# Performance work log

Measured on AMD Instinct MI355X. Metric: run time of the kernel, lower is better.

## Reference

```python
import jax, jax.numpy as jnp
import numpy as np


def _hard_sigmoid(x):
    # Keras ConvLSTM2D default recurrent_activation
    return jnp.clip(0.2 * x + 0.5, 0.0, 1.0)


def _conv(x, w):
    # NHWC input, HWIO kernel, SAME padding, stride 1
    return jax.lax.conv_general_dilated(
        x, w, (1, 1), 'SAME', dimension_numbers=('NHWC', 'HWIO', 'NHWC'))


def _convlstm(seq, h, c, k, rk, b):
    # seq: [B, T, H, W, Cin]; h, c: [B, H, W, F]
    # k: [kh, kw, Cin, 4F], rk: [kh, kw, F, 4F], b: [4F]
    def step(carry, x):
        h, c = carry
        z = _conv(x, k) + _conv(h, rk) + b  # [B,H,W,4F]
        zi, zf, zc, zo = jnp.split(z, 4, axis=-1)
        i = _hard_sigmoid(zi)
        f = _hard_sigmoid(zf)
        o = _hard_sigmoid(zo)
        c = f * c + i * jnp.tanh(zc)
        h = o * jnp.tanh(c)
        return (h, c), None
    (h, c), _ = jax.lax.scan(step, (h, c), jnp.swapaxes(seq, 0, 1))
    return h, c


def setup_inputs() -> dict:
    key = jax.random.key(0)
    ks = jax.random.split(key, 14)
    B, T, H, W, Cin, F, K = 32, 1, 64, 64, 1, 64, 3
    s = 0.05
    inp = {
        'input_': jax.random.normal(ks[0], (B, T, H, W, Cin), jnp.float32),
        'h0': jax.random.normal(ks[1], (B, H, W, F), jnp.float32) * s,
        'c0': jax.random.normal(ks[2], (B, H, W, F), jnp.float32) * s,
        'h1': jax.random.normal(ks[3], (B, H, W, F), jnp.float32) * s,
        'c1': jax.random.normal(ks[4], (B, H, W, F), jnp.float32) * s,
        'k0': jax.random.normal(ks[5], (K, K, Cin, 4 * F), jnp.float32) * s,
        'rk0': jax.random.normal(ks[6], (K, K, F, 4 * F), jnp.float32) * s,
        'b0': jnp.zeros((4 * F,), jnp.float32),
        'k1': jax.random.normal(ks[7], (K, K, F, 4 * F), jnp.float32) * s,
        'rk1': jax.random.normal(ks[8], (K, K, F, 4 * F), jnp.float32) * s,
        'b1': jnp.zeros((4 * F,), jnp.float32),
        'cw': jax.random.normal(ks[9], (1, 1, F, 1), jnp.float32) * s,
        'cb': jnp.zeros((1,), jnp.float32),
    }
    return inp


def reference(input_, h0, c0, h1, c1, k0, rk0, b0, k1, rk1, b1, cw, cb):
    # Layer 0 consumes the input frame sequence (T=1)
    h0n, c0n = _convlstm(input_, h0, c0, k0, rk0, b0)
    # Layer 1 consumes layer-0's last hidden state as its (length-1) input
    h1n, c1n = _convlstm(h0n[:, None], h1, c1, k1, rk1, b1)
    frames = _conv(h1n, cw) + cb  # 1x1 conv head -> [B,H,W,1]
    return frames, h0n, c0n, h1n, c1n
```

## Files before the change

kernel.cpp:

```cpp
#include <hip/hip_runtime.h>
#include <hip/hip_bf16.h>

typedef short s16;
typedef __attribute__((ext_vector_type(8))) short bf16x8;
typedef __attribute__((ext_vector_type(4))) float f32x4;

__device__ __forceinline__ s16 f2bf(float f) {
  unsigned u = __builtin_bit_cast(unsigned, f);
  unsigned r = (u + 0x7FFFu + ((u >> 16) & 1u)) >> 16;
  return (s16)r;
}

__device__ __forceinline__ float hsig(float x) {
  return fminf(fmaxf(0.2f * x + 0.5f, 0.0f), 1.0f);
}

__global__ void wprep_kernel(const float* __restrict__ rk0, const float* __restrict__ k1,
                             const float* __restrict__ rk1, const float* __restrict__ k0,
                             s16* __restrict__ w0q, s16* __restrict__ w1q,
                             s16* __restrict__ w2q, s16* __restrict__ k0t) {
  int idx = blockIdx.x * 256 + threadIdx.x;
  const int n1 = 9 * 2 * 4 * 4 * 512;
  if (idx < 3 * n1) {
    int which = idx / n1;
    int i = idx - which * n1;
    int e    = i & 7;
    int lane = (i >> 3) & 63;
    int g    = (i >> 9) & 3;
    int j    = (i >> 11) & 3;
    int k    = (i >> 13) & 1;
    int tap  = i >> 14;
    int l15 = lane & 15, l4 = lane >> 4;
    int ic = k * 32 + l4 * 8 + e;
    int oc = j * 64 + g * 16 + l15;
    const float* src = (which == 0) ? rk0 : (which == 1) ? k1 : rk1;
    s16* dst = (which == 0) ? w0q : (which == 1) ? w1q : w2q;
    dst[i] = f2bf(src[(tap * 64 + ic) * 256 + oc]);
  } else if (idx < 3 * n1 + 8192) {
    int r = idx - 3 * n1;
    int kk = r & 31;
    int oc = r >> 5;
    k0t[r] = (kk < 9) ? f2bf(k0[kk * 256 + oc]) : (s16)0;
  }
}

#define PXS 66
#define ROWSZ (PXS * 64)
#define ASZ (4 * ROWSZ)

template <bool F32>
__device__ __forceinline__ bf16x8 load_conv8(const void* src, long off) {
  if constexpr (F32) {
    const float* p = (const float*)src + off;
    float4 v0 = *reinterpret_cast<const float4*>(p);
    float4 v1 = *reinterpret_cast<const float4*>(p + 4);
    bf16x8 r;
    r[0] = f2bf(v0.x); r[1] = f2bf(v0.y); r[2] = f2bf(v0.z); r[3] = f2bf(v0.w);
    r[4] = f2bf(v1.x); r[5] = f2bf(v1.y); r[6] = f2bf(v1.z); r[7] = f2bf(v1.w);
    return r;
  } else {
    return *reinterpret_cast<const bf16x8*>((const s16*)src + off);
  }
}

template <bool F32>
__device__ __forceinline__ void stage_src(s16* a_lds, const void* src, int b, int y0, int tid) {
  #pragma unroll
  for (int i = 0; i < 4; ++i) {
    int c   = tid + i * 512;
    int row = c >> 9;
    int px  = (c >> 3) & 63;
    int cb  = c & 7;
    int y   = y0 - 1 + row;
    int xp  = px + 1;
    bf16x8 v = {};
    if ((unsigned)y < 64u)
      v = load_conv8<F32>(src, ((long)(b * 64 + y) * 64 + px) * 64 + cb * 8);
    *reinterpret_cast<bf16x8*>(a_lds + (row * PXS + xp) * 64 + ((cb ^ (xp & 7)) * 8)) = v;
  }
  if (tid < 64) {
    int row = tid >> 4;
    int xp  = ((tid >> 3) & 1) ? 65 : 0;
    int cb  = tid & 7;
    bf16x8 z = {};
    *reinterpret_cast<bf16x8*>(a_lds + (row * PXS + xp) * 64 + cb * 8) = z;
  }
}

template <int NSRC, bool XPATH, bool S0F32, bool S1F32>
__global__ __launch_bounds__(512, 4) void cell_kernel(
    const void* __restrict__ src0,
    const void* __restrict__ src1,
    const s16* __restrict__ w0,
    const s16* __restrict__ w1,
    const float* __restrict__ xin,
    const s16* __restrict__ k0t,
    const float* __restrict__ bias,
    const float* __restrict__ c_old,
    float* __restrict__ h_out,
    float* __restrict__ c_out,
    s16* __restrict__ hb_out)
{
  __shared__ __align__(16) s16 a_lds[NSRC * ASZ];
  __shared__ float x_lds[XPATH ? 256 : 1];

  const int tid = threadIdx.x;
  const int b  = blockIdx.x >> 5;
  const int y0 = (blockIdx.x & 31) << 1;

  stage_src<S0F32>(a_lds, src0, b, y0, tid);
  if (NSRC == 2) stage_src<S1F32>(a_lds + ASZ, src1, b, y0, tid);
  if (XPATH) {
    if (tid < 256) {
      int row = tid >> 6, px = tid & 63;
      int y = y0 - 1 + row;
      x_lds[tid] = ((unsigned)y < 64u) ? xin[(b * 64 + y) * 64 + px] : 0.0f;
    }
  }
  __syncthreads();

  const int wave = tid >> 6;
  const int lane = tid & 63;
  const int g    = wave & 3;
  const int mh   = wave >> 2;
  const int l15  = lane & 15;
  const int l4   = lane >> 4;

  constexpr int NST = NSRC * 18;

  f32x4 acc[4][4] = {};

  if (XPATH) {
    bf16x8 bx[4];
    #pragma unroll
    for (int j = 0; j < 4; ++j) {
      int oc = j * 64 + g * 16 + l15;
      bx[j] = *reinterpret_cast<const bf16x8*>(k0t + oc * 32 + l4 * 8);
    }
    #pragma unroll
    for (int m = 0; m < 4; ++m) {
      int px = m * 16 + l15;
      bf16x8 ax = {};
      #pragma unroll
      for (int j = 0; j < 8; ++j) {
        int t = l4 * 8 + j;
        if (t < 9) {
          int dyt = t / 3, dxt = t - dyt * 3;
          int xx = px + dxt - 1;
          float xv = ((unsigned)xx < 64u) ? x_lds[(mh + dyt) * 64 + xx] : 0.0f;
          ax[j] = f2bf(xv);
        }
      }
      #pragma unroll
      for (int j = 0; j < 4; ++j)
        acc[m][j] = __builtin_amdgcn_mfma_f32_16x16x32_bf16(ax, bx[j], acc[m][j], 0, 0, 0);
    }
  }

  const int wl_off = g * 512 + lane * 8;
  auto loadW = [&](bf16x8 (&wf)[4], int u) {
    int si = (NSRC == 2 && u >= 18) ? 1 : 0;
    const s16* wp = (si ? w1 : w0) + (u - 18 * si) * 8192 + wl_off;
    #pragma unroll
    for (int j = 0; j < 4; ++j)
      wf[j] = *reinterpret_cast<const bf16x8*>(wp + j * 2048);
  };

  auto doStage = [&](const bf16x8 (&wf)[4], int u) {
    int si = (NSRC == 2 && u >= 18) ? 1 : 0;
    int uu = u - 18 * si;
    int tap = uu >> 1, kk = uu & 1;
    int dy = tap / 3, dx = tap - dy * 3;
    const char* lb = (const char*)a_lds + (si * ASZ + (mh + dy) * ROWSZ) * 2;
    #pragma unroll
    for (int m = 0; m < 4; ++m) {
      int xq   = m * 16 + l15 + dx;
      int boff = xq * 128 + (((kk << 6) | (l4 << 4)) ^ ((xq & 7) << 4));
      bf16x8 a = *reinterpret_cast<const bf16x8*>(lb + boff);
      #pragma unroll
      for (int j = 0; j < 4; ++j)
        acc[m][j] = __builtin_amdgcn_mfma_f32_16x16x32_bf16(a, wf[j], acc[m][j], 0, 0, 0);
    }
  };

  bf16x8 wfA[4], wfB[4];
  loadW(wfA, 0);
  loadW(wfB, 1);
  #pragma unroll
  for (int u = 0; u < NST; u += 2) {
    doStage(wfA, u);
    if (u + 2 < NST) loadW(wfA, u + 2);
    doStage(wfB, u + 1);
    if (u + 3 < NST) loadW(wfB, u + 3);
  }

  float bi[4];
  #pragma unroll
  for (int j = 0; j < 4; ++j) bi[j] = bias[j * 64 + g * 16 + l15];

  const int pix_base = b * 4096 + y0 * 64;
  const int f = g * 16 + l15;
  #pragma unroll
  for (int m = 0; m < 4; ++m) {
    #pragma unroll
    for (int r = 0; r < 4; ++r) {
      int pl = mh * 64 + m * 16 + l4 * 4 + r;
      int off = (pix_base + pl) * 64 + f;
      float zi = acc[m][0][r] + bi[0];
      float zf = acc[m][1][r] + bi[1];
      float zc = acc[m][2][r] + bi[2];
      float zo = acc[m][3][r] + bi[3];
      float ig = hsig(zi), fg = hsig(zf), og = hsig(zo);
      float cn = fg * c_old[off] + ig * tanhf(zc);
      float hn = og * tanhf(cn);
      c_out[off] = cn;
      h_out[off] = hn;
      if (hb_out) hb_out[off] = f2bf(hn);
    }
  }
}

__global__ void frames_kernel(const float* __restrict__ h, const float* __restrict__ cw,
                              const float* __restrict__ cbp, float* __restrict__ out) {
  int tid = blockIdx.x * 256 + threadIdx.x;
  int p  = tid >> 2;
  int fc = (tid & 3) * 16;
  const float4* hp = reinterpret_cast<const float4*>(h + p * 64 + fc);
  const float4* wp = reinterpret_cast<const float4*>(cw + fc);
  float s = 0.0f;
  #pragma unroll
  for (int i = 0; i < 4; ++i) {
    float4 v = hp[i];
    float4 w = wp[i];
    s += v.x * w.x + v.y * w.y + v.z * w.z + v.w * w.w;
  }
  s += __shfl_xor(s, 1);
  s += __shfl_xor(s, 2);
  if ((tid & 3) == 0) out[p] = s + cbp[0];
}

extern "C" void kernel_launch(void* const* d_in, const int* in_sizes, int n_in,
                              void* d_out, int out_size, void* d_ws, size_t ws_size,
                              hipStream_t stream) {
  const float* x   = (const float*)d_in[0];
  const float* h0  = (const float*)d_in[1];
  const float* c0  = (const float*)d_in[2];
  const float* h1  = (const float*)d_in[3];
  const float* c1  = (const float*)d_in[4];
  const float* k0  = (const float*)d_in[5];
  const float* rk0 = (const float*)d_in[6];
  const float* b0  = (const float*)d_in[7];
  const float* k1  = (const float*)d_in[8];
  const float* rk1 = (const float*)d_in[9];
  const float* b1  = (const float*)d_in[10];
  const float* cw  = (const float*)d_in[11];
  const float* cbp = (const float*)d_in[12];

  float* out    = (float*)d_out;
  float* frames = out;
  float* h0n    = out + 131072;
  float* c0n    = out + 131072 + 8388608;
  float* h1n    = out + 131072 + 2 * 8388608;
  float* c1n    = out + 131072 + 3 * 8388608;

  char* ws = (char*)d_ws;
  const size_t SZ_H = 16777216;
  s16* h0nb = (s16*)(ws + 0 * SZ_H);
  s16* w0q  = (s16*)(ws + 1 * SZ_H);
  s16* w1q  = (s16*)(ws + 1 * SZ_H + 1 * 294912);
  s16* w2q  = (s16*)(ws + 1 * SZ_H + 2 * 294912);
  s16* k0t  = (s16*)(ws + 1 * SZ_H + 3 * 294912);

  wprep_kernel<<<1760, 256, 0, stream>>>(rk0, k1, rk1, k0, w0q, w1q, w2q, k0t);

  cell_kernel<1, true, true, false><<<1024, 512, 0, stream>>>(
      h0, nullptr, w0q, nullptr, x, k0t, b0, c0, h0n, c0n, h0nb);

  cell_kernel<2, false, false, true><<<1024, 512, 0, stream>>>(
      h0nb, h1, w1q, w2q, nullptr, nullptr, b1, c1, h1n, c1n, nullptr);

  frames_kernel<<<2048, 256, 0, stream>>>(h1n, cw, cbp, frames);
}
```

Measured before the change: 206.5 us.

## Switch cell conv GEMM to 32x32x16 MFMA with remapped wave tiling

```diff
diff --git a/kernel.cpp b/kernel.cpp
--- a/kernel.cpp
+++ b/kernel.cpp
@@ -3,7 +3,7 @@
 
 typedef short s16;
 typedef __attribute__((ext_vector_type(8))) short bf16x8;
-typedef __attribute__((ext_vector_type(4))) float f32x4;
+typedef __attribute__((ext_vector_type(16))) float f32x16;
 
 __device__ __forceinline__ s16 f2bf(float f) {
   unsigned u = __builtin_bit_cast(unsigned, f);
@@ -20,26 +20,27 @@
                              s16* __restrict__ w0q, s16* __restrict__ w1q,
                              s16* __restrict__ w2q, s16* __restrict__ k0t) {
   int idx = blockIdx.x * 256 + threadIdx.x;
-  const int n1 = 9 * 2 * 4 * 4 * 512;
+  const int n1 = 18 * 8192;
   if (idx < 3 * n1) {
     int which = idx / n1;
     int i = idx - which * n1;
     int e    = i & 7;
     int lane = (i >> 3) & 63;
-    int g    = (i >> 9) & 3;
-    int j    = (i >> 11) & 3;
-    int k    = (i >> 13) & 1;
-    int tap  = i >> 14;
-    int l15 = lane & 15, l4 = lane >> 4;
-    int ic = k * 32 + l4 * 8 + e;
-    int oc = j * 64 + g * 16 + l15;
+    int g2   = (i >> 9) & 1;
+    int j    = (i >> 10) & 3;
+    int k16  = (i >> 12) & 1;
+    int t2   = i >> 13;
+    int l31 = lane & 31, lh = lane >> 5;
+    int tap = t2 >> 1, k32 = t2 & 1;
+    int ic = k32 * 32 + k16 * 16 + lh * 8 + e;
+    int oc = j * 64 + g2 * 32 + l31;
     const float* src = (which == 0) ? rk0 : (which == 1) ? k1 : rk1;
     s16* dst = (which == 0) ? w0q : (which == 1) ? w1q : w2q;
     dst[i] = f2bf(src[(tap * 64 + ic) * 256 + oc]);
-  } else if (idx < 3 * n1 + 8192) {
+  } else if (idx < 3 * n1 + 4096) {
     int r = idx - 3 * n1;
-    int kk = r & 31;
-    int oc = r >> 5;
+    int kk = r & 15;
+    int oc = r >> 4;
     k0t[r] = (kk < 9) ? f2bf(k0[kk * 256 + oc]) : (s16)0;
   }
 }
@@ -121,102 +122,94 @@
 
   const int wave = tid >> 6;
   const int lane = tid & 63;
-  const int g    = wave & 3;
-  const int mh   = wave >> 2;
-  const int l15  = lane & 15;
-  const int l4   = lane >> 4;
-
-  constexpr int NST = NSRC * 18;
-
-  f32x4 acc[4][4] = {};
+  const int g2   = wave & 1;
+  const int mq   = wave >> 1;
+  const int l31  = lane & 31;
+  const int lh   = lane >> 5;
+  const int xbase = (mq & 1) * 32 + l31;
+  const int rowb  = mq >> 1;
+
+  constexpr int NSTEP = NSRC * 36;
+
+  f32x16 acc[4] = {};
 
   if (XPATH) {
-    bf16x8 bx[4];
     #pragma unroll
     for (int j = 0; j < 4; ++j) {
-      int oc = j * 64 + g * 16 + l15;
-      bx[j] = *reinterpret_cast<const bf16x8*>(k0t + oc * 32 + l4 * 8);
-    }
-    #pragma unroll
-    for (int m = 0; m < 4; ++m) {
-      int px = m * 16 + l15;
+      int oc = j * 64 + g2 * 32 + l31;
+      bf16x8 bx = *reinterpret_cast<const bf16x8*>(k0t + oc * 16 + lh * 8);
       bf16x8 ax = {};
       #pragma unroll
-      for (int j = 0; j < 8; ++j) {
-        int t = l4 * 8 + j;
+      for (int e = 0; e < 8; ++e) {
+        int t = lh * 8 + e;
         if (t < 9) {
           int dyt = t / 3, dxt = t - dyt * 3;
-          int xx = px + dxt - 1;
-          float xv = ((unsigned)xx < 64u) ? x_lds[(mh + dyt) * 64 + xx] : 0.0f;
-          ax[j] = f2bf(xv);
+          int xx = xbase + dxt - 1;
+          float xv = ((unsigned)xx < 64u) ? x_lds[(rowb + dyt) * 64 + xx] : 0.0f;
+          ax[e] = f2bf(xv);
         }
       }
-      #pragma unroll
-      for (int j = 0; j < 4; ++j)
-        acc[m][j] = __builtin_amdgcn_mfma_f32_16x16x32_bf16(ax, bx[j], acc[m][j], 0, 0, 0);
+      acc[j] = __builtin_amdgcn_mfma_f32_32x32x16_bf16(ax, bx, acc[j], 0, 0, 0);
     }
   }
 
-  const int wl_off = g * 512 + lane * 8;
-  auto loadW = [&](bf16x8 (&wf)[4], int u) {
+  const int wl_off = g2 * 512 + lane * 8;
+  auto loadW = [&](bf16x8 (&wf)[4], int s) {
+    int u = s >> 1, k16 = s & 1;
     int si = (NSRC == 2 && u >= 18) ? 1 : 0;
-    const s16* wp = (si ? w1 : w0) + (u - 18 * si) * 8192 + wl_off;
+    const s16* wp = (si ? w1 : w0) + (u - 18 * si) * 8192 + k16 * 4096 + wl_off;
     #pragma unroll
     for (int j = 0; j < 4; ++j)
-      wf[j] = *reinterpret_cast<const bf16x8*>(wp + j * 2048);
+      wf[j] = *reinterpret_cast<const bf16x8*>(wp + j * 1024);
   };
 
-  auto doStage = [&](const bf16x8 (&wf)[4], int u) {
+  auto doStep = [&](const bf16x8 (&wf)[4], int s) {
+    int u = s >> 1, k16 = s & 1;
     int si = (NSRC == 2 && u >= 18) ? 1 : 0;
     int uu = u - 18 * si;
-    int tap = uu >> 1, kk = uu & 1;
+    int tap = uu >> 1, k32 = uu & 1;
     int dy = tap / 3, dx = tap - dy * 3;
-    const char* lb = (const char*)a_lds + (si * ASZ + (mh + dy) * ROWSZ) * 2;
+    int xq = xbase + dx;
+    int cb = k32 * 4 + k16 * 2 + lh;
+    int boff = xq * 128 + ((cb ^ (xq & 7)) * 16);
+    const char* lb = (const char*)a_lds + (si * ASZ + (rowb + dy) * ROWSZ) * 2;
+    bf16x8 a = *reinterpret_cast<const bf16x8*>(lb + boff);
     #pragma unroll
-    for (int m = 0; m < 4; ++m) {
-      int xq   = m * 16 + l15 + dx;
-      int boff = xq * 128 + (((kk << 6) | (l4 << 4)) ^ ((xq & 7) << 4));
-      bf16x8 a = *reinterpret_cast<const bf16x8*>(lb + boff);
-      #pragma unroll
-      for (int j = 0; j < 4; ++j)
-        acc[m][j] = __builtin_amdgcn_mfma_f32_16x16x32_bf16(a, wf[j], acc[m][j], 0, 0, 0);
-    }
+    for (int j = 0; j < 4; ++j)
+      acc[j] = __builtin_amdgcn_mfma_f32_32x32x16_bf16(a, wf[j], acc[j], 0, 0, 0);
   };
 
   bf16x8 wfA[4], wfB[4];
   loadW(wfA, 0);
   loadW(wfB, 1);
   #pragma unroll
-  for (int u = 0; u < NST; u += 2) {
-    doStage(wfA, u);
-    if (u + 2 < NST) loadW(wfA, u + 2);
-    doStage(wfB, u + 1);
-    if (u + 3 < NST) loadW(wfB, u + 3);
+  for (int s = 0; s < NSTEP; s += 2) {
+    doStep(wfA, s);
+    if (s + 2 < NSTEP) loadW(wfA, s + 2);
+    doStep(wfB, s + 1);
+    if (s + 3 < NSTEP) loadW(wfB, s + 3);
   }
 
   float bi[4];
   #pragma unroll
-  for (int j = 0; j < 4; ++j) bi[j] = bias[j * 64 + g * 16 + l15];
+  for (int j = 0; j < 4; ++j) bi[j] = bias[j * 64 + g2 * 32 + l31];
 
   const int pix_base = b * 4096 + y0 * 64;
-  const int f = g * 16 + l15;
-  #pragma unroll
-  for (int m = 0; m < 4; ++m) {
-    #pragma unroll
-    for (int r = 0; r < 4; ++r) {
-      int pl = mh * 64 + m * 16 + l4 * 4 + r;
-      int off = (pix_base + pl) * 64 + f;
-      float zi = acc[m][0][r] + bi[0];
-      float zf = acc[m][1][r] + bi[1];
-      float zc = acc[m][2][r] + bi[2];
-      float zo = acc[m][3][r] + bi[3];
-      float ig = hsig(zi), fg = hsig(zf), og = hsig(zo);
-      float cn = fg * c_old[off] + ig * tanhf(zc);
-      float hn = og * tanhf(cn);
-      c_out[off] = cn;
-      h_out[off] = hn;
-      if (hb_out) hb_out[off] = f2bf(hn);
-    }
+  const int f = g2 * 32 + l31;
+  #pragma unroll
+  for (int r = 0; r < 16; ++r) {
+    int pxl = (r & 3) + 8 * (r >> 2) + 4 * lh;
+    int off = (pix_base + mq * 32 + pxl) * 64 + f;
+    float zi = acc[0][r] + bi[0];
+    float zf = acc[1][r] + bi[1];
+    float zc = acc[2][r] + bi[2];
+    float zo = acc[3][r] + bi[3];
+    float ig = hsig(zi), fg = hsig(zf), og = hsig(zo);
+    float cn = fg * c_old[off] + ig * tanhf(zc);
+    float hn = og * tanhf(cn);
+    c_out[off] = cn;
+    h_out[off] = hn;
+    if (hb_out) hb_out[off] = f2bf(hn);
   }
 }
 
@@ -271,7 +264,7 @@
   s16* w2q  = (s16*)(ws + 1 * SZ_H + 2 * 294912);
   s16* k0t  = (s16*)(ws + 1 * SZ_H + 3 * 294912);
 
-  wprep_kernel<<<1760, 256, 0, stream>>>(rk0, k1, rk1, k0, w0q, w1q, w2q, k0t);
+  wprep_kernel<<<1744, 256, 0, stream>>>(rk0, k1, rk1, k0, w0q, w1q, w2q, k0t);
 
   cell_kernel<1, true, true, false><<<1024, 512, 0, stream>>>(
       h0, nullptr, w0q, nullptr, x, k0t, b0, c0, h0n, c0n, h0nb);
```

Result: slower. 288.7 us (+39.8%).

## Split cell tile across 16 waves with halved accumulators and rolled loop

Applied to the files above, without the earlier changes.

```diff
diff --git a/kernel.cpp b/kernel.cpp
--- a/kernel.cpp
+++ b/kernel.cpp
@@ -20,7 +20,7 @@
                              s16* __restrict__ w0q, s16* __restrict__ w1q,
                              s16* __restrict__ w2q, s16* __restrict__ k0t) {
   int idx = blockIdx.x * 256 + threadIdx.x;
-  const int n1 = 9 * 2 * 4 * 4 * 512;
+  const int n1 = 18 * 8192;
   if (idx < 3 * n1) {
     int which = idx / n1;
     int i = idx - which * n1;
@@ -66,8 +66,8 @@
 template <bool F32>
 __device__ __forceinline__ void stage_src(s16* a_lds, const void* src, int b, int y0, int tid) {
   #pragma unroll
-  for (int i = 0; i < 4; ++i) {
-    int c   = tid + i * 512;
+  for (int i = 0; i < 2; ++i) {
+    int c   = tid + i * 1024;
     int row = c >> 9;
     int px  = (c >> 3) & 63;
     int cb  = c & 7;
@@ -88,7 +88,7 @@
 }
 
 template <int NSRC, bool XPATH, bool S0F32, bool S1F32>
-__global__ __launch_bounds__(512, 4) void cell_kernel(
+__global__ __launch_bounds__(1024, 8) void cell_kernel(
     const void* __restrict__ src0,
     const void* __restrict__ src1,
     const s16* __restrict__ w0,
@@ -121,34 +121,36 @@
 
   const int wave = tid >> 6;
   const int lane = tid & 63;
-  const int g    = wave & 3;
-  const int mh   = wave >> 2;
+  const int gg   = wave & 3;
+  const int pp   = wave >> 2;
   const int l15  = lane & 15;
   const int l4   = lane >> 4;
+  const int rb   = pp >> 1;
+  const int xbase = (pp & 1) * 32 + l15;
 
   constexpr int NST = NSRC * 18;
 
-  f32x4 acc[4][4] = {};
+  f32x4 acc[2][4] = {};
 
   if (XPATH) {
     bf16x8 bx[4];
     #pragma unroll
     for (int j = 0; j < 4; ++j) {
-      int oc = j * 64 + g * 16 + l15;
+      int oc = j * 64 + gg * 16 + l15;
       bx[j] = *reinterpret_cast<const bf16x8*>(k0t + oc * 32 + l4 * 8);
     }
     #pragma unroll
-    for (int m = 0; m < 4; ++m) {
-      int px = m * 16 + l15;
+    for (int m = 0; m < 2; ++m) {
+      int px = xbase + m * 16;
       bf16x8 ax = {};
       #pragma unroll
-      for (int j = 0; j < 8; ++j) {
-        int t = l4 * 8 + j;
+      for (int e = 0; e < 8; ++e) {
+        int t = l4 * 8 + e;
         if (t < 9) {
           int dyt = t / 3, dxt = t - dyt * 3;
           int xx = px + dxt - 1;
-          float xv = ((unsigned)xx < 64u) ? x_lds[(mh + dyt) * 64 + xx] : 0.0f;
-          ax[j] = f2bf(xv);
+          float xv = ((unsigned)xx < 64u) ? x_lds[(rb + dyt) * 64 + xx] : 0.0f;
+          ax[e] = f2bf(xv);
         }
       }
       #pragma unroll
@@ -157,54 +159,47 @@
     }
   }
 
-  const int wl_off = g * 512 + lane * 8;
-  auto loadW = [&](bf16x8 (&wf)[4], int u) {
-    int si = (NSRC == 2 && u >= 18) ? 1 : 0;
-    const s16* wp = (si ? w1 : w0) + (u - 18 * si) * 8192 + wl_off;
-    #pragma unroll
-    for (int j = 0; j < 4; ++j)
-      wf[j] = *reinterpret_cast<const bf16x8*>(wp + j * 2048);
-  };
-
-  auto doStage = [&](const bf16x8 (&wf)[4], int u) {
-    int si = (NSRC == 2 && u >= 18) ? 1 : 0;
-    int uu = u - 18 * si;
+  const int wl_off = gg * 512 + lane * 8;
+  #pragma unroll 1
+  for (int u = 0; u < NST; ++u) {
+    int si  = (NSRC == 2 && u >= 18) ? 1 : 0;
+    int uu  = u - 18 * si;
     int tap = uu >> 1, kk = uu & 1;
-    int dy = tap / 3, dx = tap - dy * 3;
-    const char* lb = (const char*)a_lds + (si * ASZ + (mh + dy) * ROWSZ) * 2;
-    #pragma unroll
-    for (int m = 0; m < 4; ++m) {
-      int xq   = m * 16 + l15 + dx;
-      int boff = xq * 128 + (((kk << 6) | (l4 << 4)) ^ ((xq & 7) << 4));
-      bf16x8 a = *reinterpret_cast<const bf16x8*>(lb + boff);
-      #pragma unroll
-      for (int j = 0; j < 4; ++j)
-        acc[m][j] = __builtin_amdgcn_mfma_f32_16x16x32_bf16(a, wf[j], acc[m][j], 0, 0, 0);
-    }
-  };
-
-  bf16x8 wfA[4], wfB[4];
-  loadW(wfA, 0);
-  loadW(wfB, 1);
-  #pragma unroll
-  for (int u = 0; u < NST; u += 2) {
-    doStage(wfA, u);
-    if (u + 2 < NST) loadW(wfA, u + 2);
-    doStage(wfB, u + 1);
-    if (u + 3 < NST) loadW(wfB, u + 3);
+    int dy  = (tap * 11) >> 5;
+    int dx  = tap - dy * 3;
+    const char* lb = (const char*)a_lds + (si * ASZ + (rb + dy) * ROWSZ) * 2;
+    int xq  = xbase + dx;
+    int swz = (((kk << 2) | l4) ^ (xq & 7)) << 4;
+    bf16x8 a0 = *reinterpret_cast<const bf16x8*>(lb + xq * 128 + swz);
+    bf16x8 a1 = *reinterpret_cast<const bf16x8*>(lb + (xq + 16) * 128 + swz);
+    const s16* wp = (si ? w1 : w0) + uu * 8192 + wl_off;
+    bf16x8 wf0 = *reinterpret_cast<const bf16x8*>(wp);
+    bf16x8 wf1 = *reinterpret_cast<const bf16x8*>(wp + 2048);
+    bf16x8 wf2 = *reinterpret_cast<const bf16x8*>(wp + 4096);
+    bf16x8 wf3 = *reinterpret_cast<const bf16x8*>(wp + 6144);
+    __builtin_amdgcn_s_setprio(1);
+    acc[0][0] = __builtin_amdgcn_mfma_f32_16x16x32_bf16(a0, wf0, acc[0][0], 0, 0, 0);
+    acc[0][1] = __builtin_amdgcn_mfma_f32_16x16x32_bf16(a0, wf1, acc[0][1], 0, 0, 0);
+    acc[0][2] = __builtin_amdgcn_mfma_f32_16x16x32_bf16(a0, wf2, acc[0][2], 0, 0, 0);
+    acc[0][3] = __builtin_amdgcn_mfma_f32_16x16x32_bf16(a0, wf3, acc[0][3], 0, 0, 0);
+    acc[1][0] = __builtin_amdgcn_mfma_f32_16x16x32_bf16(a1, wf0, acc[1][0], 0, 0, 0);
+    acc[1][1] = __builtin_amdgcn_mfma_f32_16x16x32_bf16(a1, wf1, acc[1][1], 0, 0, 0);
+    acc[1][2] = __builtin_amdgcn_mfma_f32_16x16x32_bf16(a1, wf2, acc[1][2], 0, 0, 0);
+    acc[1][3] = __builtin_amdgcn_mfma_f32_16x16x32_bf16(a1, wf3, acc[1][3], 0, 0, 0);
+    __builtin_amdgcn_s_setprio(0);
   }
 
   float bi[4];
   #pragma unroll
-  for (int j = 0; j < 4; ++j) bi[j] = bias[j * 64 + g * 16 + l15];
+  for (int j = 0; j < 4; ++j) bi[j] = bias[j * 64 + gg * 16 + l15];
 
   const int pix_base = b * 4096 + y0 * 64;
-  const int f = g * 16 + l15;
-  #pragma unroll
-  for (int m = 0; m < 4; ++m) {
+  const int f = gg * 16 + l15;
+  #pragma unroll
+  for (int m = 0; m < 2; ++m) {
     #pragma unroll
     for (int r = 0; r < 4; ++r) {
-      int pl = mh * 64 + m * 16 + l4 * 4 + r;
+      int pl = pp * 32 + m * 16 + l4 * 4 + r;
       int off = (pix_base + pl) * 64 + f;
       float zi = acc[m][0][r] + bi[0];
       float zf = acc[m][1][r] + bi[1];
@@ -273,10 +268,10 @@
 
   wprep_kernel<<<1760, 256, 0, stream>>>(rk0, k1, rk1, k0, w0q, w1q, w2q, k0t);
 
-  cell_kernel<1, true, true, false><<<1024, 512, 0, stream>>>(
+  cell_kernel<1, true, true, false><<<1024, 1024, 0, stream>>>(
       h0, nullptr, w0q, nullptr, x, k0t, b0, c0, h0n, c0n, h0nb);
 
-  cell_kernel<2, false, false, true><<<1024, 512, 0, stream>>>(
+  cell_kernel<2, false, false, true><<<1024, 1024, 0, stream>>>(
       h0nb, h1, w1q, w2q, nullptr, nullptr, b1, c1, h1n, c1n, nullptr);
 
   frames_kernel<<<2048, 256, 0, stream>>>(h1n, cw, cbp, frames);
```

After: 220.8 us. +6.9%, slower.

## Process four output rows per block to amortize weight loads and halo

Applied to the files above, without the earlier changes.

```diff
diff --git a/kernel.cpp b/kernel.cpp
--- a/kernel.cpp
+++ b/kernel.cpp
@@ -20,7 +20,7 @@
                              s16* __restrict__ w0q, s16* __restrict__ w1q,
                              s16* __restrict__ w2q, s16* __restrict__ k0t) {
   int idx = blockIdx.x * 256 + threadIdx.x;
-  const int n1 = 9 * 2 * 4 * 4 * 512;
+  const int n1 = 18 * 8192;
   if (idx < 3 * n1) {
     int which = idx / n1;
     int i = idx - which * n1;
@@ -46,7 +46,7 @@
 
 #define PXS 66
 #define ROWSZ (PXS * 64)
-#define ASZ (4 * ROWSZ)
+#define ASZ (6 * ROWSZ)
 
 template <bool F32>
 __device__ __forceinline__ bf16x8 load_conv8(const void* src, long off) {
@@ -66,7 +66,7 @@
 template <bool F32>
 __device__ __forceinline__ void stage_src(s16* a_lds, const void* src, int b, int y0, int tid) {
   #pragma unroll
-  for (int i = 0; i < 4; ++i) {
+  for (int i = 0; i < 6; ++i) {
     int c   = tid + i * 512;
     int row = c >> 9;
     int px  = (c >> 3) & 63;
@@ -78,7 +78,7 @@
       v = load_conv8<F32>(src, ((long)(b * 64 + y) * 64 + px) * 64 + cb * 8);
     *reinterpret_cast<bf16x8*>(a_lds + (row * PXS + xp) * 64 + ((cb ^ (xp & 7)) * 8)) = v;
   }
-  if (tid < 64) {
+  if (tid < 96) {
     int row = tid >> 4;
     int xp  = ((tid >> 3) & 1) ? 65 : 0;
     int cb  = tid & 7;
@@ -88,7 +88,7 @@
 }
 
 template <int NSRC, bool XPATH, bool S0F32, bool S1F32>
-__global__ __launch_bounds__(512, 4) void cell_kernel(
+__global__ __launch_bounds__(512, 2) void cell_kernel(
     const void* __restrict__ src0,
     const void* __restrict__ src1,
     const s16* __restrict__ w0,
@@ -102,16 +102,16 @@
     s16* __restrict__ hb_out)
 {
   __shared__ __align__(16) s16 a_lds[NSRC * ASZ];
-  __shared__ float x_lds[XPATH ? 256 : 1];
+  __shared__ float x_lds[XPATH ? 384 : 1];
 
   const int tid = threadIdx.x;
-  const int b  = blockIdx.x >> 5;
-  const int y0 = (blockIdx.x & 31) << 1;
+  const int b  = blockIdx.x >> 4;
+  const int y0 = (blockIdx.x & 15) << 2;
 
   stage_src<S0F32>(a_lds, src0, b, y0, tid);
   if (NSRC == 2) stage_src<S1F32>(a_lds + ASZ, src1, b, y0, tid);
   if (XPATH) {
-    if (tid < 256) {
+    if (tid < 384) {
       int row = tid >> 6, px = tid & 63;
       int y = y0 - 1 + row;
       x_lds[tid] = ((unsigned)y < 64u) ? xin[(b * 64 + y) * 64 + px] : 0.0f;
@@ -128,7 +128,7 @@
 
   constexpr int NST = NSRC * 18;
 
-  f32x4 acc[4][4] = {};
+  f32x4 acc[8][4] = {};
 
   if (XPATH) {
     bf16x8 bx[4];
@@ -138,17 +138,18 @@
       bx[j] = *reinterpret_cast<const bf16x8*>(k0t + oc * 32 + l4 * 8);
     }
     #pragma unroll
-    for (int m = 0; m < 4; ++m) {
-      int px = m * 16 + l15;
+    for (int m = 0; m < 8; ++m) {
+      int rb = 2 * mh + (m >> 2);
+      int px = (m & 3) * 16 + l15;
       bf16x8 ax = {};
       #pragma unroll
-      for (int j = 0; j < 8; ++j) {
-        int t = l4 * 8 + j;
+      for (int e = 0; e < 8; ++e) {
+        int t = l4 * 8 + e;
         if (t < 9) {
           int dyt = t / 3, dxt = t - dyt * 3;
           int xx = px + dxt - 1;
-          float xv = ((unsigned)xx < 64u) ? x_lds[(mh + dyt) * 64 + xx] : 0.0f;
-          ax[j] = f2bf(xv);
+          float xv = ((unsigned)xx < 64u) ? x_lds[(rb + dyt) * 64 + xx] : 0.0f;
+          ax[e] = f2bf(xv);
         }
       }
       #pragma unroll
@@ -171,16 +172,23 @@
     int uu = u - 18 * si;
     int tap = uu >> 1, kk = uu & 1;
     int dy = tap / 3, dx = tap - dy * 3;
-    const char* lb = (const char*)a_lds + (si * ASZ + (mh + dy) * ROWSZ) * 2;
-    #pragma unroll
-    for (int m = 0; m < 4; ++m) {
-      int xq   = m * 16 + l15 + dx;
-      int boff = xq * 128 + (((kk << 6) | (l4 << 4)) ^ ((xq & 7) << 4));
-      bf16x8 a = *reinterpret_cast<const bf16x8*>(lb + boff);
+    const char* sb = (const char*)a_lds + si * (ASZ * 2);
+    bf16x8 af[8];
+    #pragma unroll
+    for (int m = 0; m < 8; ++m) {
+      int row  = 2 * mh + (m >> 2) + dy;
+      int xq   = (m & 3) * 16 + l15 + dx;
+      int boff = xq * 128 + ((((kk << 2) | l4) ^ (xq & 7)) << 4);
+      af[m] = *reinterpret_cast<const bf16x8*>(sb + row * (ROWSZ * 2) + boff);
+    }
+    __builtin_amdgcn_s_setprio(1);
+    #pragma unroll
+    for (int m = 0; m < 8; ++m) {
       #pragma unroll
       for (int j = 0; j < 4; ++j)
-        acc[m][j] = __builtin_amdgcn_mfma_f32_16x16x32_bf16(a, wf[j], acc[m][j], 0, 0, 0);
-    }
+        acc[m][j] = __builtin_amdgcn_mfma_f32_16x16x32_bf16(af[m], wf[j], acc[m][j], 0, 0, 0);
+    }
+    __builtin_amdgcn_s_setprio(0);
   };
 
   bf16x8 wfA[4], wfB[4];
@@ -201,10 +209,10 @@
   const int pix_base = b * 4096 + y0 * 64;
   const int f = g * 16 + l15;
   #pragma unroll
-  for (int m = 0; m < 4; ++m) {
+  for (int m = 0; m < 8; ++m) {
     #pragma unroll
     for (int r = 0; r < 4; ++r) {
-      int pl = mh * 64 + m * 16 + l4 * 4 + r;
+      int pl = (2 * mh + (m >> 2)) * 64 + (m & 3) * 16 + l4 * 4 + r;
       int off = (pix_base + pl) * 64 + f;
       float zi = acc[m][0][r] + bi[0];
       float zf = acc[m][1][r] + bi[1];
@@ -273,10 +281,10 @@
 
   wprep_kernel<<<1760, 256, 0, stream>>>(rk0, k1, rk1, k0, w0q, w1q, w2q, k0t);
 
-  cell_kernel<1, true, true, false><<<1024, 512, 0, stream>>>(
+  cell_kernel<1, true, true, false><<<512, 512, 0, stream>>>(
       h0, nullptr, w0q, nullptr, x, k0t, b0, c0, h0n, c0n, h0nb);
 
-  cell_kernel<2, false, false, true><<<1024, 512, 0, stream>>>(
+  cell_kernel<2, false, false, true><<<512, 512, 0, stream>>>(
       h0nb, h1, w1q, w2q, nullptr, nullptr, b1, c1, h1n, c1n, nullptr);
 
   frames_kernel<<<2048, 256, 0, stream>>>(h1n, cw, cbp, frames);
```

After: 242.6 us. 17.5% more time.
